# Kernel tuning notes

Hardware: AMD Instinct MI355X
Metric: run time of the kernel (lower is better)

The kernel has to match this reference:

```python
import jax, jax.numpy as jnp
import numpy as np

B, SQ, SKV, D = 4, 2048, 2048, 2048
NEG = -1e9


def setup_inputs() -> dict:
    key = jax.random.key(0)
    ks = jax.random.split(key, 7)
    x = jax.random.normal(ks[0], (B, SKV, D), dtype=jnp.float32)
    enc_q = jax.random.normal(ks[1], (B, SQ, D), dtype=jnp.float32)
    enc_k = jax.random.normal(ks[2], (B, SKV, D), dtype=jnp.float32)
    i_mask = jax.random.bernoulli(ks[3], 0.1, (B, SQ, SKV))  # True -> masked
    s = 1.0 / np.sqrt(D)
    Wq = jax.random.normal(ks[4], (D, D), dtype=jnp.float32) * s
    Wk = jax.random.normal(ks[5], (D, D), dtype=jnp.float32) * s
    Wv = jax.random.normal(ks[6], (D, D), dtype=jnp.float32) * s
    return {"x": x, "enc_q": enc_q, "enc_k": enc_k, "i_mask": i_mask,
            "Wq": Wq, "Wk": Wk, "Wv": Wv}


def reference(x, enc_q, enc_k, i_mask, Wq, Wk, Wv):
    # Bias-free linear projections (nn.Linear: y = x @ W^T)
    q = jnp.einsum('bsd,ed->bse', enc_q, Wq)   # [B,SQ,D]
    k = jnp.einsum('bsd,ed->bse', enc_k, Wk)   # [B,SKV,D]
    v = jnp.einsum('bsd,ed->bse', x, Wv)       # [B,SKV,D]
    scale = 1.0 / jnp.sqrt(jnp.asarray(q.shape[-1], q.dtype))
    scores = jnp.einsum('bqd,bkd->bqk', q, k) * scale  # [B,SQ,SKV]
    scores = jnp.where(i_mask, jnp.asarray(NEG, scores.dtype), scores)
    attn = jax.nn.softmax(scores, axis=-1)
    return jnp.einsum('bqk,bkd->bqd', attn, v)  # [B,SQ,D]
```

## Files before the change

### kernel.cpp

```cpp
#include <hip/hip_runtime.h>
#include <stdint.h>

typedef short  short8  __attribute__((ext_vector_type(8)));
typedef unsigned short ushort8 __attribute__((ext_vector_type(8)));
typedef unsigned short ushort4v __attribute__((ext_vector_type(4)));
typedef float  f32x4   __attribute__((ext_vector_type(4)));

#define BB  4
#define SQL 2048
#define SKL 2048
#define NEGV -1e9f
#define AS1 __attribute__((address_space(1)))
#define AS3 __attribute__((address_space(3)))

__device__ __forceinline__ unsigned short f2bf(float f){
  union { float f; uint32_t u; } x; x.f = f;
  return (unsigned short)((x.u + 0x7FFFu + ((x.u >> 16) & 1u)) >> 16);
}
__device__ __forceinline__ float bf2f(unsigned short h){
  union { uint32_t u; float f; } x; x.u = ((uint32_t)h) << 16;
  return x.f;
}

#define BARR() __builtin_amdgcn_s_barrier()
#define SBAR() __builtin_amdgcn_s_barrier()
#define LGKM0() asm volatile("s_waitcnt lgkmcnt(0)" ::: "memory")
#define VMW(N)  asm volatile("s_waitcnt vmcnt(" #N ")"   ::: "memory")
#define PRIO1 __builtin_amdgcn_s_setprio(1)
#define PRIO0 __builtin_amdgcn_s_setprio(0)

__global__ void mask_detect(const uint8_t* __restrict__ m, int* __restrict__ cnt){
  const long n4 = (long)BB * SQL * SKL / 4;
  long idx  = (long)blockIdx.x * blockDim.x + threadIdx.x;
  long step = (long)gridDim.x * blockDim.x;
  int c0 = 0, c1 = 0, c2 = 0;
  for (long i4 = idx; i4 < n4; i4 += step){
    uchar4 b = ((const uchar4*)m)[i4];
    c0 += (b.y != 0) + (b.z != 0) + (b.w != 0);
    c1 += (b.x > 1) + (b.y > 1) + (b.z > 1) + (b.w > 1);
    c2 += (b.y != 0);
  }
  #pragma unroll
  for (int o = 32; o >= 1; o >>= 1){
    c0 += __shfl_xor(c0, o); c1 += __shfl_xor(c1, o); c2 += __shfl_xor(c2, o);
  }
  if ((threadIdx.x & 63) == 0){
    atomicAdd(&cnt[0], c0); atomicAdd(&cnt[1], c1); atomicAdd(&cnt[2], c2);
  }
}

__global__ __launch_bounds__(256)
void cvt4(const float* __restrict__ s0, const float* __restrict__ s1,
          const float* __restrict__ s2, const float* __restrict__ s3,
          unsigned short* __restrict__ d0, unsigned short* __restrict__ d1,
          unsigned short* __restrict__ d2, unsigned short* __restrict__ d3)
{
  const long total = 6815744;
  for (long c = (long)blockIdx.x * blockDim.x + threadIdx.x; c < total;
       c += (long)gridDim.x * blockDim.x){
    const float* s; unsigned short* d; long off;
    if      (c < 2097152){ s = s0; d = d0; off = c; }
    else if (c < 4194304){ s = s1; d = d1; off = c - 2097152; }
    else if (c < 6291456){ s = s2; d = d2; off = c - 4194304; }
    else                 { s = s3; d = d3; off = c - 6291456; }
    f32x4 a = ((const f32x4*)s)[off * 2];
    f32x4 b = ((const f32x4*)s)[off * 2 + 1];
    ushort8 w;
    #pragma unroll
    for (int j = 0; j < 4; ++j){ w[j] = f2bf(a[j]); w[j + 4] = f2bf(b[j]); }
    ((ushort8*)d)[off] = w;
  }
}

__global__ __launch_bounds__(256)
void transpose_cvt2(const float* __restrict__ s0, const float* __restrict__ s1,
                    unsigned short* __restrict__ d0, unsigned short* __restrict__ d1)
{
  __shared__ float t[32][33];
  const float* s = blockIdx.z ? s1 : s0;
  unsigned short* d = blockIdx.z ? d1 : d0;
  const long bx = blockIdx.x * 32, by = blockIdx.y * 32;
  const int tx = threadIdx.x & 31, ty = threadIdx.x >> 5;
  #pragma unroll
  for (int j = 0; j < 4; ++j)
    t[ty + j * 8][tx] = s[(by + ty + j * 8) * 2048 + bx + tx];
  __syncthreads();
  #pragma unroll
  for (int j = 0; j < 4; ++j)
    d[(bx + ty + j * 8) * 2048 + by + tx] = f2bf(t[tx][ty + j * 8]);
}

__device__ __forceinline__ void xcd_decode(int& bx, int& by, int& bz){
  const int gx = gridDim.x, gy = gridDim.y;
  const int nwg = gx * gy * gridDim.z;
  const int lid = blockIdx.x + gx * (blockIdx.y + gy * blockIdx.z);
  const int sw  = (lid & 7) * (nwg >> 3) + (lid >> 3);
  bx = sw % gx;
  const int t = sw / gx;
  by = t % gy;
  bz = t / gy;
}

template<int EPI>
__device__ __forceinline__ void gemm256_body(
    const unsigned short* __restrict__ Ag, const unsigned short* __restrict__ Bg,
    void* __restrict__ Cb, const void* __restrict__ mask, const int* __restrict__ cnt,
    int bz, long Cbs, long tm, long tn, float scale,
    unsigned short (&lA)[2][16384], unsigned short (&lB)[2][16384])
{
  constexpr int LD = 2048;
  const int tid = threadIdx.x, lane = tid & 63, wid = tid >> 6;
  const int wm = wid >> 2, wn = wid & 3;
  const int l15 = lane & 15, l16 = lane >> 4;

  f32x4 acc[2][2][4][2] = {};
  short8 aF[4][2];
  short8 bF[2][2][2];

  auto stageA = [&](int buf, int half, int k){
    const unsigned short* s = Ag + (tm + half * 128) * LD + k;
    unsigned short* d = lA[buf] + half * 8192;
    #pragma unroll
    for (int l = 0; l < 2; ++l){
      const int idx = l * 512 + tid;
      const int r   = idx >> 3;
      const int gsw = (idx & 7) ^ (r & 7);
      __builtin_amdgcn_global_load_lds((const AS1 void*)(s + r * LD + gsw * 8),
                                       (AS3 void*)(d + idx * 8), 16, 0, 0);
    }
  };
  auto stageB = [&](int buf, int half, int k){
    const unsigned short* s = Bg + (tn + half * 128) * LD + k;
    unsigned short* d = lB[buf] + half * 8192;
    #pragma unroll
    for (int l = 0; l < 2; ++l){
      const int idx = l * 512 + tid;
      const int r   = idx >> 3;
      const int gsw = (idx & 7) ^ (r & 7);
      __builtin_amdgcn_global_load_lds((const AS1 void*)(s + r * LD + gsw * 8),
                                       (AS3 void*)(d + idx * 8), 16, 0, 0);
    }
  };

  #define RD_A(BUF, QM)                                                       \
    _Pragma("unroll")                                                         \
    for (int mr = 0; mr < 4; ++mr)                                            \
      _Pragma("unroll")                                                       \
      for (int ks = 0; ks < 2; ++ks){                                         \
        const int r = (QM) * 128 + wm * 64 + mr * 16 + l15;                   \
        const int g = ks * 4 + l16;                                           \
        aF[mr][ks] = *(const short8*)&lA[(BUF)][(r * 8 + (g ^ (r & 7))) * 8]; \
      }
  #define RD_B(BUF, QN)                                                       \
    _Pragma("unroll")                                                         \
    for (int nr = 0; nr < 2; ++nr)                                            \
      _Pragma("unroll")                                                       \
      for (int ks = 0; ks < 2; ++ks){                                         \
        const int c = (QN) * 128 + wn * 32 + nr * 16 + l15;                   \
        const int g = ks * 4 + l16;                                           \
        bF[QN][nr][ks] = *(const short8*)&lB[(BUF)][(c * 8 + (g ^ (c & 7))) * 8]; \
      }
  #define MFMA16(QM, QN)                                                      \
    _Pragma("unroll")                                                         \
    for (int mr = 0; mr < 4; ++mr)                                            \
      _Pragma("unroll")                                                       \
      for (int nr = 0; nr < 2; ++nr)                                          \
        _Pragma("unroll")                                                     \
        for (int ks = 0; ks < 2; ++ks)                                        \
          acc[QM][QN][mr][nr] = __builtin_amdgcn_mfma_f32_16x16x32_bf16(      \
              aF[mr][ks], bF[QN][nr][ks], acc[QM][QN][mr][nr], 0, 0, 0);

  #define KTILE_MAIN(BUF, KNXT)                                               \
  {                                                                           \
    RD_A(BUF, 0); RD_B(BUF, 0);                                               \
    stageA((BUF) ^ 1, 0, (KNXT));                                             \
    BARR(); LGKM0();                                                          \
    PRIO1; MFMA16(0, 0); PRIO0; VMW(4); BARR();                               \
    RD_B(BUF, 1);                                                             \
    stageB((BUF) ^ 1, 0, (KNXT));                                             \
    BARR(); LGKM0();                                                          \
    PRIO1; MFMA16(0, 1); PRIO0; VMW(4); BARR();                               \
    RD_A(BUF, 1);                                                             \
    stageB((BUF) ^ 1, 1, (KNXT));                                             \
    BARR(); LGKM0();                                                          \
    PRIO1; MFMA16(1, 1); PRIO0; BARR();                                       \
    stageA((BUF) ^ 1, 1, (KNXT));                                             \
    BARR();                                                                   \
    PRIO1; MFMA16(1, 0); PRIO0; VMW(2); BARR();                               \
  }
  #define KTILE_LAST(BUF)                                                     \
  {                                                                           \
    RD_A(BUF, 0); RD_B(BUF, 0);                                               \
    BARR(); LGKM0();                                                          \
    PRIO1; MFMA16(0, 0); PRIO0; VMW(2); BARR();                               \
    RD_B(BUF, 1);                                                             \
    BARR(); LGKM0();                                                          \
    PRIO1; MFMA16(0, 1); PRIO0; VMW(0); BARR();                               \
    RD_A(BUF, 1);                                                             \
    BARR(); LGKM0();                                                          \
    PRIO1; MFMA16(1, 1); PRIO0; BARR();                                       \
    PRIO1; MFMA16(1, 0); PRIO0;                                               \
  }

  stageA(0, 0, 0);
  stageB(0, 0, 0);
  stageB(0, 1, 0);
  stageA(0, 1, 0);
  VMW(4); BARR();

  for (int it = 0; it < 15; ++it){
    KTILE_MAIN(0, (2 * it + 1) * 64);
    KTILE_MAIN(1, (2 * it + 2) * 64);
  }
  KTILE_MAIN(0, 31 * 64);
  KTILE_LAST(1);

  const int colo = l15, rowg = l16 * 4;
  if constexpr (EPI == 0){
    unsigned short* C = (unsigned short*)Cb + (long)bz * Cbs;
    #pragma unroll
    for (int qm = 0; qm < 2; ++qm)
      #pragma unroll
      for (int qn = 0; qn < 2; ++qn)
        #pragma unroll
        for (int mr = 0; mr < 4; ++mr)
          #pragma unroll
          for (int j = 0; j < 4; ++j){
            const long row = tm + qm * 128 + wm * 64 + mr * 16 + rowg + j;
            unsigned short* cr = C + row * LD + tn + qn * 128 + wn * 32 + colo;
            #pragma unroll
            for (int nr = 0; nr < 2; ++nr) cr[nr * 16] = f2bf(acc[qm][qn][mr][nr][j] * scale);
          }
  } else if constexpr (EPI == 2){
    float* C = (float*)Cb + (long)bz * Cbs;
    #pragma unroll
    for (int qm = 0; qm < 2; ++qm)
      #pragma unroll
      for (int qn = 0; qn < 2; ++qn)
        #pragma unroll
        for (int mr = 0; mr < 4; ++mr)
          #pragma unroll
          for (int j = 0; j < 4; ++j){
            const long row = tm + qm * 128 + wm * 64 + mr * 16 + rowg + j;
            float* cr = C + row * LD + tn + qn * 128 + wn * 32 + colo;
            #pragma unroll
            for (int nr = 0; nr < 2; ++nr) cr[nr * 16] = acc[qm][qn][mr][nr][j];
          }
  } else {
    const int a0 = cnt[0], a1 = cnt[1], a2 = cnt[2];
    const int mmode = (a1 == 0) ? (a0 > 1000 ? 0 : 1) : (a2 > 1000 ? 2 : 3);
    unsigned short* C = (unsigned short*)Cb + (long)bz * Cbs;
    const long mbase = (long)bz * SQL * SKL;
    #pragma unroll
    for (int qm = 0; qm < 2; ++qm)
      #pragma unroll
      for (int qn = 0; qn < 2; ++qn)
        #pragma unroll
        for (int mr = 0; mr < 4; ++mr)
          #pragma unroll
          for (int j = 0; j < 4; ++j){
            const long row = tm + qm * 128 + wm * 64 + mr * 16 + rowg + j;
            #pragma unroll
            for (int nr = 0; nr < 2; ++nr){
              const long col = tn + qn * 128 + wn * 32 + nr * 16 + colo;
              const long midx = mbase + row * SKL + col;
              bool msk;
              if (mmode == 0)      msk = ((const uint8_t*)mask)[midx] != 0;
              else if (mmode == 1) msk = ((const int*)mask)[midx] != 0;
              else if (mmode == 2) msk = ((const unsigned short*)mask)[midx] != 0;
              else                 msk = ((const uint32_t*)mask)[midx] != 0;
              float vv = acc[qm][qn][mr][nr][j] * scale;
              if (msk) vv = NEGV;
              C[row * SKL + col] = f2bf(vv);
            }
          }
  }
  #undef RD_A
  #undef RD_B
  #undef MFMA16
  #undef KTILE_MAIN
  #undef KTILE_LAST
}

template<int EPI>
__global__ __launch_bounds__(512, 2)
void gemm256(const unsigned short* __restrict__ A, const unsigned short* __restrict__ B,
             void* __restrict__ Cb, const void* __restrict__ mask,
             const int* __restrict__ cnt, long Abs, long Bbs, long Cbs, float scale)
{
  __shared__ unsigned short lA[2][16384];
  __shared__ unsigned short lB[2][16384];
  int bx, by, bz; xcd_decode(bx, by, bz);
  gemm256_body<EPI>(A + (long)bz * Abs, B + (long)bz * Bbs, Cb, mask, cnt, bz, Cbs,
                    (long)by * 256, (long)bx * 256, scale, lA, lB);
}

__global__ __launch_bounds__(512, 2)
void gemm256_proj2(const unsigned short* A0, const unsigned short* A1,
                   const unsigned short* B0, const unsigned short* B1,
                   void* C0, void* C1)
{
  __shared__ unsigned short lA[2][16384];
  __shared__ unsigned short lB[2][16384];
  int bx, by, bz; xcd_decode(bx, by, bz);
  const int sec = bz >> 2, b = bz & 3;
  const long NN = (long)SQL * 2048;
  const unsigned short* Av = sec ? A1 : A0;
  const unsigned short* Bv = sec ? B1 : B0;
  void*                 Cv = sec ? C1 : C0;
  const long Abs = sec ? 0 : NN;
  const long Bbs = sec ? NN : 0;
  gemm256_body<0>(Av + (long)b * Abs, Bv + (long)b * Bbs, Cv, nullptr, nullptr, b, NN,
                  (long)by * 256, (long)bx * 256, 1.f, lA, lB);
}

template<int AMODE, int BMODE, int EPI>
__device__ __forceinline__ void gemm_body(
    const void* __restrict__ Av, const void* __restrict__ Bv,
    void* __restrict__ Cb, const void* __restrict__ mask, const int* __restrict__ cnt,
    int bz, long Abs, long Bbs, long Cbs, long tm, long tn, float scale,
    int koff, int klen,
    unsigned short (*lA)[4096], unsigned short (*lB)[4096])
{
  constexpr int LD = 2048;
  const int tid = threadIdx.x, lane = tid & 63, wave = tid >> 6;
  const int wr = wave >> 1, wc = wave & 1;
  const int c0 = tid, c1 = tid + 256;
  const int r0 = c0 >> 2, q0 = (c0 & 3) * 8;
  const int r1 = c1 >> 2, q1 = (c1 & 3) * 8;

  const unsigned short* A16 = (const unsigned short*)Av + (long)bz * Abs;
  const unsigned short* B16 = (const unsigned short*)Bv + (long)bz * Bbs;
  const float*          A32 = (const float*)Av + (long)bz * Abs;
  const float*          B32 = (const float*)Bv + (long)bz * Bbs;

  f32x4 acc[4][4] = {};
  f32x4 sA[4], sB[4];

  auto issueA = [&](int buf, int kk){
    if constexpr (AMODE == 0){
      __builtin_amdgcn_global_load_lds((const AS1 void*)(A16 + (tm + r0) * LD + q0 + kk),
                                       (AS3 void*)(lA[buf] + c0 * 8), 16, 0, 0);
      __builtin_amdgcn_global_load_lds((const AS1 void*)(A16 + (tm + r1) * LD + q1 + kk),
                                       (AS3 void*)(lA[buf] + c1 * 8), 16, 0, 0);
    } else {
      sA[0] = *(const f32x4*)(A32 + (tm + r0) * LD + q0 + kk);
      sA[1] = *(const f32x4*)(A32 + (tm + r0) * LD + q0 + kk + 4);
      sA[2] = *(const f32x4*)(A32 + (tm + r1) * LD + q1 + kk);
      sA[3] = *(const f32x4*)(A32 + (tm + r1) * LD + q1 + kk + 4);
    }
  };
  auto issueB = [&](int buf, int kk){
    if constexpr (BMODE == 0){
      __builtin_amdgcn_global_load_lds((const AS1 void*)(B16 + (tn + r0) * LD + q0 + kk),
                                       (AS3 void*)(lB[buf] + c0 * 8), 16, 0, 0);
      __builtin_amdgcn_global_load_lds((const AS1 void*)(B16 + (tn + r1) * LD + q1 + kk),
                                       (AS3 void*)(lB[buf] + c1 * 8), 16, 0, 0);
    } else {
      sB[0] = *(const f32x4*)(B32 + (tn + r0) * LD + q0 + kk);
      sB[1] = *(const f32x4*)(B32 + (tn + r0) * LD + q0 + kk + 4);
      sB[2] = *(const f32x4*)(B32 + (tn + r1) * LD + q1 + kk);
      sB[3] = *(const f32x4*)(B32 + (tn + r1) * LD + q1 + kk + 4);
    }
  };
  auto writeA = [&](int buf){
    if constexpr (AMODE == 1){
      ushort8 w0, w1;
      #pragma unroll
      for (int j = 0; j < 4; ++j){
        w0[j] = f2bf(sA[0][j]); w0[j + 4] = f2bf(sA[1][j]);
        w1[j] = f2bf(sA[2][j]); w1[j + 4] = f2bf(sA[3][j]);
      }
      *(ushort8*)(lA[buf] + c0 * 8) = w0;
      *(ushort8*)(lA[buf] + c1 * 8) = w1;
    }
  };
  auto writeB = [&](int buf){
    if constexpr (BMODE == 1){
      ushort8 w0, w1;
      #pragma unroll
      for (int j = 0; j < 4; ++j){
        w0[j] = f2bf(sB[0][j]); w0[j + 4] = f2bf(sB[1][j]);
        w1[j] = f2bf(sB[2][j]); w1[j + 4] = f2bf(sB[3][j]);
      }
      *(ushort8*)(lB[buf] + c0 * 8) = w0;
      *(ushort8*)(lB[buf] + c1 * 8) = w1;
    }
  };
  auto computeTile = [&](int buf){
    short8 aF[4], bF[4];
    #pragma unroll
    for (int m = 0; m < 4; ++m)
      aF[m] = *(const short8*)(lA[buf] + (wr * 64 + m * 16 + (lane & 15)) * 32 + (lane >> 4) * 8);
    #pragma unroll
    for (int n = 0; n < 4; ++n)
      bF[n] = *(const short8*)(lB[buf] + (wc * 64 + n * 16 + (lane & 15)) * 32 + (lane >> 4) * 8);
    #pragma unroll
    for (int m = 0; m < 4; ++m)
      #pragma unroll
      for (int n = 0; n < 4; ++n)
        acc[m][n] = __builtin_amdgcn_mfma_f32_16x16x32_bf16(aF[m], bF[n], acc[m][n], 0, 0, 0);
  };

  issueA(0, koff); issueB(0, koff); writeA(0); writeB(0);
  __syncthreads();
  int cur = 0;
  for (int k0 = koff; k0 < koff + klen - 32; k0 += 32){
    issueA(cur ^ 1, k0 + 32);
    issueB(cur ^ 1, k0 + 32);
    computeTile(cur);
    writeA(cur ^ 1); writeB(cur ^ 1);
    __syncthreads();
    cur ^= 1;
  }
  computeTile(cur);

  const int colo = lane & 15, rowg = (lane >> 4) * 4;
  if constexpr (EPI == 0){
    unsigned short* C = (unsigned short*)Cb + (long)bz * Cbs;
    #pragma unroll
    for (int m = 0; m < 4; ++m)
      #pragma unroll
      for (int j = 0; j < 4; ++j){
        const long row = tm + wr * 64 + m * 16 + rowg + j;
        unsigned short* cr = C + row * LD + tn + wc * 64 + colo;
        #pragma unroll
        for (int n = 0; n < 4; ++n) cr[n * 16] = f2bf(acc[m][n][j] * scale);
      }
  } else if constexpr (EPI == 2){
    float* C = (float*)Cb + (long)bz * Cbs;
    #pragma unroll
    for (int m = 0; m < 4; ++m)
      #pragma unroll
      for (int j = 0; j < 4; ++j){
        const long row = tm + wr * 64 + m * 16 + rowg + j;
        float* cr = C + row * LD + tn + wc * 64 + colo;
        #pragma unroll
        for (int n = 0; n < 4; ++n) cr[n * 16] = acc[m][n][j];
      }
  } else {
    const int a0 = cnt[0], a1 = cnt[1], a2 = cnt[2];
    const int mmode = (a1 == 0) ? (a0 > 1000 ? 0 : 1) : (a2 > 1000 ? 2 : 3);
    unsigned short* C = (unsigned short*)Cb + (long)bz * Cbs;
    const long mbase = (long)bz * SQL * SKL;
    #pragma unroll
    for (int m = 0; m < 4; ++m)
      #pragma unroll
      for (int j = 0; j < 4; ++j){
        const long row = tm + wr * 64 + m * 16 + rowg + j;
        #pragma unroll
        for (int n = 0; n < 4; ++n){
          const long col = tn + wc * 64 + n * 16 + colo;
          const long midx = mbase + row * SKL + col;
          bool msk;
          if (mmode == 0)      msk = ((const uint8_t*)mask)[midx] != 0;
          else if (mmode == 1) msk = ((const int*)mask)[midx] != 0;
          else if (mmode == 2) msk = ((const unsigned short*)mask)[midx] != 0;
          else                 msk = ((const uint32_t*)mask)[midx] != 0;
          float vv = acc[m][n][j] * scale;
          if (msk) vv = NEGV;
          C[row * SKL + col] = f2bf(vv);
        }
      }
  }
}

template<int AMODE, int BMODE, int EPI>
__global__ __launch_bounds__(256, 2)
void gemm_nt(const void* __restrict__ Abv, const void* __restrict__ Bbv,
             void* __restrict__ Cb, const void* __restrict__ mask,
             const int* __restrict__ cnt,
             long Abs, long Bbs, long Cbs, float scale)
{
  __shared__ unsigned short lA[2][4096];
  __shared__ unsigned short lB[2][4096];
  int bx, by, bz; xcd_decode(bx, by, bz);
  gemm_body<AMODE, BMODE, EPI>(Abv, Bbv, Cb, mask, cnt, bz, Abs, Bbs, Cbs,
                               (long)by * 128, (long)bx * 128, scale, 0, 2048, lA, lB);
}

__global__ __launch_bounds__(256, 2)
void gemm_splitk(const unsigned short* __restrict__ A, const unsigned short* __restrict__ B,
                 float* __restrict__ Cp)
{
  __shared__ unsigned short lA[2][4096];
  __shared__ unsigned short lB[2][4096];
  int bx, by, bz; xcd_decode(bx, by, bz);
  gemm_body<0, 0, 2>(A, B, Cp + (long)bz * 4194304, nullptr, nullptr, 0, 0, 0, 4194304,
                     (long)by * 128, (long)bx * 128, 1.f, bz * 512, 512, lA, lB);
}

__global__ __launch_bounds__(256)
void mt_reduce(const float* __restrict__ Cp, unsigned short* __restrict__ Mt, float scale){
  for (long c = (long)blockIdx.x * blockDim.x + threadIdx.x; c < 1048576;
       c += (long)gridDim.x * blockDim.x){
    f32x4 a = ((const f32x4*)Cp)[c];
    f32x4 b = ((const f32x4*)(Cp + 4194304))[c];
    f32x4 d = ((const f32x4*)(Cp + 8388608))[c];
    f32x4 e = ((const f32x4*)(Cp + 12582912))[c];
    ushort4v w;
    #pragma unroll
    for (int j = 0; j < 4; ++j) w[j] = f2bf((a[j] + b[j] + d[j] + e[j]) * scale);
    ((ushort4v*)Mt)[c] = w;
  }
}

template<int MODE>
__global__ __launch_bounds__(256, 2)
void gemm_proj3(const void* A0, const void* A1, const void* A2,
                const void* B0, const void* B1, const void* B2,
                void* C0, void* C1, void* C2)
{
  __shared__ unsigned short lA[2][4096];
  __shared__ unsigned short lB[2][4096];
  int bx, by, bz; xcd_decode(bx, by, bz);
  const int sec = bz >> 2, b = bz & 3;
  const long NN = (long)SQL * 2048;
  const void* Av = sec == 0 ? A0 : sec == 1 ? A1 : A2;
  const void* Bv = sec == 0 ? B0 : sec == 1 ? B1 : B2;
  void*       Cv = sec == 0 ? C0 : sec == 1 ? C1 : C2;
  const long Abs = (sec == 2) ? 0 : NN;
  const long Bbs = (sec == 2) ? NN : 0;
  gemm_body<MODE, MODE, 0>(Av, Bv, Cv, nullptr, nullptr, b, Abs, Bbs, NN,
                           (long)by * 128, (long)bx * 128, 1.f, 0, 2048, lA, lB);
}

__global__ __launch_bounds__(256, 4)
void softmax_rows(const unsigned short* __restrict__ S, unsigned short* __restrict__ P){
  const long row = blockIdx.x;
  const int t = threadIdx.x;
  ushort8 u = *((const ushort8*)(S + row * SKL) + t);
  float v[8];
  #pragma unroll
  for (int j = 0; j < 8; ++j) v[j] = bf2f(u[j]);
  float mx = v[0];
  #pragma unroll
  for (int j = 1; j < 8; ++j) mx = fmaxf(mx, v[j]);
  #pragma unroll
  for (int o = 32; o >= 1; o >>= 1) mx = fmaxf(mx, __shfl_xor(mx, o));
  __shared__ float red[8];
  const int wv = t >> 6, ln = t & 63;
  if (ln == 0) red[wv] = mx;
  __syncthreads();
  mx = fmaxf(fmaxf(red[0], red[1]), fmaxf(red[2], red[3]));
  float e[8], sum = 0.f;
  #pragma unroll
  for (int j = 0; j < 8; ++j){ e[j] = exp2f((v[j] - mx) * 1.4426950408889634f); sum += e[j]; }
  #pragma unroll
  for (int o = 32; o >= 1; o >>= 1) sum += __shfl_xor(sum, o);
  if (ln == 0) red[4 + wv] = sum;
  __syncthreads();
  sum = red[4] + red[5] + red[6] + red[7];
  const float inv = 1.0f / sum;
  ushort8 o8;
  #pragma unroll
  for (int j = 0; j < 8; ++j) o8[j] = f2bf(e[j] * inv);
  *((ushort8*)(P + row * SKL) + t) = o8;
}

extern "C" void kernel_launch(void* const* d_in, const int* in_sizes, int n_in,
                              void* d_out, int out_size, void* d_ws, size_t ws_size,
                              hipStream_t stream)
{
  (void)in_sizes; (void)n_in; (void)out_size;
  const void* x    = d_in[0];
  const void* encq = d_in[1];
  const void* enck = d_in[2];
  const void* imsk = d_in[3];
  const void* Wq   = d_in[4];
  const void* Wk   = d_in[5];
  const void* Wv   = d_in[6];

  uint8_t* ws = (uint8_t*)d_ws;
  int* cnt = (int*)ws;
  const long NN = (long)2048 * 2048;
  const float scale = 0.022097086912079608f;

  hipMemsetAsync(cnt, 0, 4096, stream);
  mask_detect<<<256, 256, 0, stream>>>((const uint8_t*)imsk, cnt);

  const size_t FULL_NEED = 4096 + 4ull * 33554432 + 4ull * 8388608;
  if (ws_size >= FULL_NEED){
    unsigned short* xb  = (unsigned short*)(ws + 4096);
    unsigned short* qb  = xb  + 16777216;
    unsigned short* kb  = qb  + 16777216;
    unsigned short* Wvb = kb  + 16777216;
    unsigned short* WqT = Wvb + 4194304;
    unsigned short* WkT = WqT + 4194304;
    unsigned short* Mt  = WkT + 4194304;
    unsigned short* Vt  = Mt  + 4194304;
    unsigned short* U   = (unsigned short*)d_out;
    unsigned short* S   = U + 16777216;
    unsigned short* P   = qb;

    cvt4<<<2048, 256, 0, stream>>>((const float*)x, (const float*)encq, (const float*)enck,
                                   (const float*)Wv, xb, qb, kb, Wvb);
    transpose_cvt2<<<dim3(64, 64, 2), 256, 0, stream>>>((const float*)Wq, (const float*)Wk,
                                                        WqT, WkT);
    gemm_splitk<<<dim3(16, 16, 4), 256, 0, stream>>>(WkT, WqT, (float*)d_out);
    mt_reduce<<<1024, 256, 0, stream>>>((const float*)d_out, Mt, scale);
    gemm256_proj2<<<dim3(8, 8, 8), 512, 0, stream>>>(qb, Wvb, Mt, xb, U, Vt);
    gemm256<1><<<dim3(8, 8, BB), 512, 0, stream>>>(U, kb, S, imsk, cnt, NN, NN, NN, 1.f);
    softmax_rows<<<BB * SQL, 256, 0, stream>>>(S, P);
    gemm256<2><<<dim3(8, 8, BB), 512, 0, stream>>>(P, Vt, d_out, nullptr, cnt, NN, NN, NN, 1.f);
  } else {
    unsigned short* Q  = (unsigned short*)(ws + 4096);
    unsigned short* Kp = Q  + 16777216;
    unsigned short* Vt = Kp + 16777216;
    unsigned short* P  = Q;
    unsigned short* S;
    const size_t need = 4096 + 4ull * 33554432;
    if (ws_size >= need) S = Vt + 16777216;
    else                 S = (unsigned short*)d_out;

    gemm_proj3<1><<<dim3(16, 16, 12), 256, 0, stream>>>(encq, enck, Wv, Wq, Wk, x, Q, Kp, Vt);
    gemm_nt<0, 0, 1><<<dim3(16, 16, BB), 256, 0, stream>>>(Q, Kp, S, imsk, cnt, NN, NN, NN, scale);
    softmax_rows<<<BB * SQL, 256, 0, stream>>>(S, P);
    gemm_nt<0, 0, 2><<<dim3(16, 16, BB), 256, 0, stream>>>(P, Vt, d_out, nullptr, cnt, NN, NN, NN, 1.f);
  }
}
```

Measured before the change: 515.9 us.

## Move mask application into softmax and merge conversion kernels into one launch

Mask application moves out of the score-GEMM epilogue, which did scattered byte loads per element, and into the softmax kernel, which now reads the mask with vectorized loads per row. The GEMM epilogue becomes a plain bf16 store. The convert and transpose kernels are merged into a single prep launch to save one kernel launch. The mask then goes through softmax after bf16 rounding of the scores, which matches the earlier behaviour because the same NEG value is used either way.

After: 454.1 us. 1.14x faster.

```diff
diff --git a/kernel.cpp b/kernel.cpp
--- a/kernel.cpp
+++ b/kernel.cpp
@@ -23,7 +23,6 @@
 }
 
 #define BARR() __builtin_amdgcn_s_barrier()
-#define SBAR() __builtin_amdgcn_s_barrier()
 #define LGKM0() asm volatile("s_waitcnt lgkmcnt(0)" ::: "memory")
 #define VMW(N)  asm volatile("s_waitcnt vmcnt(" #N ")"   ::: "memory")
 #define PRIO1 __builtin_amdgcn_s_setprio(1)
@@ -50,44 +49,44 @@
 }
 
 __global__ __launch_bounds__(256)
-void cvt4(const float* __restrict__ s0, const float* __restrict__ s1,
+void prep(const float* __restrict__ s0, const float* __restrict__ s1,
           const float* __restrict__ s2, const float* __restrict__ s3,
           unsigned short* __restrict__ d0, unsigned short* __restrict__ d1,
-          unsigned short* __restrict__ d2, unsigned short* __restrict__ d3)
-{
-  const long total = 6815744;
-  for (long c = (long)blockIdx.x * blockDim.x + threadIdx.x; c < total;
-       c += (long)gridDim.x * blockDim.x){
-    const float* s; unsigned short* d; long off;
-    if      (c < 2097152){ s = s0; d = d0; off = c; }
-    else if (c < 4194304){ s = s1; d = d1; off = c - 2097152; }
-    else if (c < 6291456){ s = s2; d = d2; off = c - 4194304; }
-    else                 { s = s3; d = d3; off = c - 6291456; }
-    f32x4 a = ((const f32x4*)s)[off * 2];
-    f32x4 b = ((const f32x4*)s)[off * 2 + 1];
-    ushort8 w;
-    #pragma unroll
-    for (int j = 0; j < 4; ++j){ w[j] = f2bf(a[j]); w[j + 4] = f2bf(b[j]); }
-    ((ushort8*)d)[off] = w;
-  }
-}
-
-__global__ __launch_bounds__(256)
-void transpose_cvt2(const float* __restrict__ s0, const float* __restrict__ s1,
-                    unsigned short* __restrict__ d0, unsigned short* __restrict__ d1)
-{
-  __shared__ float t[32][33];
-  const float* s = blockIdx.z ? s1 : s0;
-  unsigned short* d = blockIdx.z ? d1 : d0;
-  const long bx = blockIdx.x * 32, by = blockIdx.y * 32;
-  const int tx = threadIdx.x & 31, ty = threadIdx.x >> 5;
-  #pragma unroll
-  for (int j = 0; j < 4; ++j)
-    t[ty + j * 8][tx] = s[(by + ty + j * 8) * 2048 + bx + tx];
-  __syncthreads();
-  #pragma unroll
-  for (int j = 0; j < 4; ++j)
-    d[(bx + ty + j * 8) * 2048 + by + tx] = f2bf(t[tx][ty + j * 8]);
+          unsigned short* __restrict__ d2, unsigned short* __restrict__ d3,
+          const float* __restrict__ tq, const float* __restrict__ tk,
+          unsigned short* __restrict__ dq, unsigned short* __restrict__ dk)
+{
+  if (blockIdx.x < 2048){
+    const long total = 6815744;
+    for (long c = (long)blockIdx.x * 256 + threadIdx.x; c < total; c += 2048 * 256){
+      const float* s; unsigned short* d; long off;
+      if      (c < 2097152){ s = s0; d = d0; off = c; }
+      else if (c < 4194304){ s = s1; d = d1; off = c - 2097152; }
+      else if (c < 6291456){ s = s2; d = d2; off = c - 4194304; }
+      else                 { s = s3; d = d3; off = c - 6291456; }
+      f32x4 a = ((const f32x4*)s)[off * 2];
+      f32x4 b = ((const f32x4*)s)[off * 2 + 1];
+      ushort8 w;
+      #pragma unroll
+      for (int j = 0; j < 4; ++j){ w[j] = f2bf(a[j]); w[j + 4] = f2bf(b[j]); }
+      ((ushort8*)d)[off] = w;
+    }
+  } else {
+    __shared__ float t[32][33];
+    const int j = blockIdx.x - 2048;
+    const int z = j >> 12, rem = j & 4095;
+    const float* s = z ? tk : tq;
+    unsigned short* d = z ? dk : dq;
+    const long bx = (long)(rem & 63) * 32, by = (long)(rem >> 6) * 32;
+    const int tx = threadIdx.x & 31, ty = threadIdx.x >> 5;
+    #pragma unroll
+    for (int jj = 0; jj < 4; ++jj)
+      t[ty + jj * 8][tx] = s[(by + ty + jj * 8) * 2048 + bx + tx];
+    __syncthreads();
+    #pragma unroll
+    for (int jj = 0; jj < 4; ++jj)
+      d[(bx + ty + jj * 8) * 2048 + by + tx] = f2bf(t[tx][ty + jj * 8]);
+  }
 }
 
 __device__ __forceinline__ void xcd_decode(int& bx, int& by, int& bz){
@@ -104,8 +103,7 @@
 template<int EPI>
 __device__ __forceinline__ void gemm256_body(
     const unsigned short* __restrict__ Ag, const unsigned short* __restrict__ Bg,
-    void* __restrict__ Cb, const void* __restrict__ mask, const int* __restrict__ cnt,
-    int bz, long Cbs, long tm, long tn, float scale,
+    void* __restrict__ Cb, int bz, long Cbs, long tm, long tn, float scale,
     unsigned short (&lA)[2][16384], unsigned short (&lB)[2][16384])
 {
   constexpr int LD = 2048;
@@ -231,7 +229,7 @@
             #pragma unroll
             for (int nr = 0; nr < 2; ++nr) cr[nr * 16] = f2bf(acc[qm][qn][mr][nr][j] * scale);
           }
-  } else if constexpr (EPI == 2){
+  } else {
     float* C = (float*)Cb + (long)bz * Cbs;
     #pragma unroll
     for (int qm = 0; qm < 2; ++qm)
@@ -246,34 +244,6 @@
             #pragma unroll
             for (int nr = 0; nr < 2; ++nr) cr[nr * 16] = acc[qm][qn][mr][nr][j];
           }
-  } else {
-    const int a0 = cnt[0], a1 = cnt[1], a2 = cnt[2];
-    const int mmode = (a1 == 0) ? (a0 > 1000 ? 0 : 1) : (a2 > 1000 ? 2 : 3);
-    unsigned short* C = (unsigned short*)Cb + (long)bz * Cbs;
-    const long mbase = (long)bz * SQL * SKL;
-    #pragma unroll
-    for (int qm = 0; qm < 2; ++qm)
-      #pragma unroll
-      for (int qn = 0; qn < 2; ++qn)
-        #pragma unroll
-        for (int mr = 0; mr < 4; ++mr)
-          #pragma unroll
-          for (int j = 0; j < 4; ++j){
-            const long row = tm + qm * 128 + wm * 64 + mr * 16 + rowg + j;
-            #pragma unroll
-            for (int nr = 0; nr < 2; ++nr){
-              const long col = tn + qn * 128 + wn * 32 + nr * 16 + colo;
-              const long midx = mbase + row * SKL + col;
-              bool msk;
-              if (mmode == 0)      msk = ((const uint8_t*)mask)[midx] != 0;
-              else if (mmode == 1) msk = ((const int*)mask)[midx] != 0;
-              else if (mmode == 2) msk = ((const unsigned short*)mask)[midx] != 0;
-              else                 msk = ((const uint32_t*)mask)[midx] != 0;
-              float vv = acc[qm][qn][mr][nr][j] * scale;
-              if (msk) vv = NEGV;
-              C[row * SKL + col] = f2bf(vv);
-            }
-          }
   }
   #undef RD_A
   #undef RD_B
@@ -285,13 +255,12 @@
 template<int EPI>
 __global__ __launch_bounds__(512, 2)
 void gemm256(const unsigned short* __restrict__ A, const unsigned short* __restrict__ B,
-             void* __restrict__ Cb, const void* __restrict__ mask,
-             const int* __restrict__ cnt, long Abs, long Bbs, long Cbs, float scale)
+             void* __restrict__ Cb, long Abs, long Bbs, long Cbs, float scale)
 {
   __shared__ unsigned short lA[2][16384];
   __shared__ unsigned short lB[2][16384];
   int bx, by, bz; xcd_decode(bx, by, bz);
-  gemm256_body<EPI>(A + (long)bz * Abs, B + (long)bz * Bbs, Cb, mask, cnt, bz, Cbs,
+  gemm256_body<EPI>(A + (long)bz * Abs, B + (long)bz * Bbs, Cb, bz, Cbs,
                     (long)by * 256, (long)bx * 256, scale, lA, lB);
 }
 
@@ -310,16 +279,15 @@
   void*                 Cv = sec ? C1 : C0;
   const long Abs = sec ? 0 : NN;
   const long Bbs = sec ? NN : 0;
-  gemm256_body<0>(Av + (long)b * Abs, Bv + (long)b * Bbs, Cv, nullptr, nullptr, b, NN,
+  gemm256_body<0>(Av + (long)b * Abs, Bv + (long)b * Bbs, Cv, b, NN,
                   (long)by * 256, (long)bx * 256, 1.f, lA, lB);
 }
 
 template<int AMODE, int BMODE, int EPI>
 __device__ __forceinline__ void gemm_body(
     const void* __restrict__ Av, const void* __restrict__ Bv,
-    void* __restrict__ Cb, const void* __restrict__ mask, const int* __restrict__ cnt,
-    int bz, long Abs, long Bbs, long Cbs, long tm, long tn, float scale,
-    int koff, int klen,
+    void* __restrict__ Cb, int bz, long Abs, long Bbs, long Cbs,
+    long tm, long tn, float scale, int koff, int klen,
     unsigned short (*lA)[4096], unsigned short (*lB)[4096])
 {
   constexpr int LD = 2048;
@@ -427,7 +395,7 @@
         #pragma unroll
         for (int n = 0; n < 4; ++n) cr[n * 16] = f2bf(acc[m][n][j] * scale);
       }
-  } else if constexpr (EPI == 2){
+  } else {
     float* C = (float*)Cb + (long)bz * Cbs;
     #pragma unroll
     for (int m = 0; m < 4; ++m)
@@ -438,44 +406,18 @@
         #pragma unroll
         for (int n = 0; n < 4; ++n) cr[n * 16] = acc[m][n][j];
       }
-  } else {
-    const int a0 = cnt[0], a1 = cnt[1], a2 = cnt[2];
-    const int mmode = (a1 == 0) ? (a0 > 1000 ? 0 : 1) : (a2 > 1000 ? 2 : 3);
-    unsigned short* C = (unsigned short*)Cb + (long)bz * Cbs;
-    const long mbase = (long)bz * SQL * SKL;
-    #pragma unroll
-    for (int m = 0; m < 4; ++m)
-      #pragma unroll
-      for (int j = 0; j < 4; ++j){
-        const long row = tm + wr * 64 + m * 16 + rowg + j;
-        #pragma unroll
-        for (int n = 0; n < 4; ++n){
-          const long col = tn + wc * 64 + n * 16 + colo;
-          const long midx = mbase + row * SKL + col;
-          bool msk;
-          if (mmode == 0)      msk = ((const uint8_t*)mask)[midx] != 0;
-          else if (mmode == 1) msk = ((const int*)mask)[midx] != 0;
-          else if (mmode == 2) msk = ((const unsigned short*)mask)[midx] != 0;
-          else                 msk = ((const uint32_t*)mask)[midx] != 0;
-          float vv = acc[m][n][j] * scale;
-          if (msk) vv = NEGV;
-          C[row * SKL + col] = f2bf(vv);
-        }
-      }
   }
 }
 
 template<int AMODE, int BMODE, int EPI>
 __global__ __launch_bounds__(256, 2)
 void gemm_nt(const void* __restrict__ Abv, const void* __restrict__ Bbv,
-             void* __restrict__ Cb, const void* __restrict__ mask,
-             const int* __restrict__ cnt,
-             long Abs, long Bbs, long Cbs, float scale)
+             void* __restrict__ Cb, long Abs, long Bbs, long Cbs, float scale)
 {
   __shared__ unsigned short lA[2][4096];
   __shared__ unsigned short lB[2][4096];
   int bx, by, bz; xcd_decode(bx, by, bz);
-  gemm_body<AMODE, BMODE, EPI>(Abv, Bbv, Cb, mask, cnt, bz, Abs, Bbs, Cbs,
+  gemm_body<AMODE, BMODE, EPI>(Abv, Bbv, Cb, bz, Abs, Bbs, Cbs,
                                (long)by * 128, (long)bx * 128, scale, 0, 2048, lA, lB);
 }
 
@@ -486,7 +428,7 @@
   __shared__ unsigned short lA[2][4096];
   __shared__ unsigned short lB[2][4096];
   int bx, by, bz; xcd_decode(bx, by, bz);
-  gemm_body<0, 0, 2>(A, B, Cp + (long)bz * 4194304, nullptr, nullptr, 0, 0, 0, 4194304,
+  gemm_body<0, 0, 2>(A, B, Cp + (long)bz * 4194304, 0, 0, 0, 4194304,
                      (long)by * 128, (long)bx * 128, 1.f, bz * 512, 512, lA, lB);
 }
 
@@ -505,11 +447,10 @@
   }
 }
 
-template<int MODE>
 __global__ __launch_bounds__(256, 2)
-void gemm_proj3(const void* A0, const void* A1, const void* A2,
-                const void* B0, const void* B1, const void* B2,
-                void* C0, void* C1, void* C2)
+void gemm_proj3f(const void* A0, const void* A1, const void* A2,
+                 const void* B0, const void* B1, const void* B2,
+                 void* C0, void* C1, void* C2)
 {
   __shared__ unsigned short lA[2][4096];
   __shared__ unsigned short lB[2][4096];
@@ -521,18 +462,42 @@
   void*       Cv = sec == 0 ? C0 : sec == 1 ? C1 : C2;
   const long Abs = (sec == 2) ? 0 : NN;
   const long Bbs = (sec == 2) ? NN : 0;
-  gemm_body<MODE, MODE, 0>(Av, Bv, Cv, nullptr, nullptr, b, Abs, Bbs, NN,
-                           (long)by * 128, (long)bx * 128, 1.f, 0, 2048, lA, lB);
+  gemm_body<1, 1, 0>(Av, Bv, Cv, b, Abs, Bbs, NN,
+                     (long)by * 128, (long)bx * 128, 1.f, 0, 2048, lA, lB);
 }
 
 __global__ __launch_bounds__(256, 4)
-void softmax_rows(const unsigned short* __restrict__ S, unsigned short* __restrict__ P){
+void softmax_rows(const unsigned short* __restrict__ S, const void* __restrict__ mask,
+                  const int* __restrict__ cnt, unsigned short* __restrict__ P){
   const long row = blockIdx.x;
   const int t = threadIdx.x;
+  const int a0 = cnt[0], a1 = cnt[1], a2 = cnt[2];
+  const int mmode = (a1 == 0) ? (a0 > 1000 ? 0 : 1) : (a2 > 1000 ? 2 : 3);
+
   ushort8 u = *((const ushort8*)(S + row * SKL) + t);
   float v[8];
   #pragma unroll
   for (int j = 0; j < 8; ++j) v[j] = bf2f(u[j]);
+
+  const long mb = row * SKL + (long)t * 8;
+  if (mmode == 0){
+    uchar4 m0 = ((const uchar4*)mask)[mb / 4], m1 = ((const uchar4*)mask)[mb / 4 + 1];
+    if (m0.x) v[0] = NEGV; if (m0.y) v[1] = NEGV; if (m0.z) v[2] = NEGV; if (m0.w) v[3] = NEGV;
+    if (m1.x) v[4] = NEGV; if (m1.y) v[5] = NEGV; if (m1.z) v[6] = NEGV; if (m1.w) v[7] = NEGV;
+  } else if (mmode == 1){
+    int4 m0 = ((const int4*)mask)[mb / 4], m1 = ((const int4*)mask)[mb / 4 + 1];
+    if (m0.x) v[0] = NEGV; if (m0.y) v[1] = NEGV; if (m0.z) v[2] = NEGV; if (m0.w) v[3] = NEGV;
+    if (m1.x) v[4] = NEGV; if (m1.y) v[5] = NEGV; if (m1.z) v[6] = NEGV; if (m1.w) v[7] = NEGV;
+  } else if (mmode == 2){
+    ushort8 m = ((const ushort8*)mask)[mb / 8];
+    #pragma unroll
+    for (int j = 0; j < 8; ++j) if (m[j]) v[j] = NEGV;
+  } else {
+    f32x4 m0 = ((const f32x4*)mask)[mb / 4], m1 = ((const f32x4*)mask)[mb / 4 + 1];
+    #pragma unroll
+    for (int j = 0; j < 4; ++j){ if (m0[j] != 0.f) v[j] = NEGV; if (m1[j] != 0.f) v[4 + j] = NEGV; }
+  }
+
   float mx = v[0];
   #pragma unroll
   for (int j = 1; j < 8; ++j) mx = fmaxf(mx, v[j]);
@@ -593,16 +558,15 @@
     unsigned short* S   = U + 16777216;
     unsigned short* P   = qb;
 
-    cvt4<<<2048, 256, 0, stream>>>((const float*)x, (const float*)encq, (const float*)enck,
-                                   (const float*)Wv, xb, qb, kb, Wvb);
-    transpose_cvt2<<<dim3(64, 64, 2), 256, 0, stream>>>((const float*)Wq, (const float*)Wk,
-                                                        WqT, WkT);
+    prep<<<10240, 256, 0, stream>>>((const float*)x, (const float*)encq, (const float*)enck,
+                                    (const float*)Wv, xb, qb, kb, Wvb,
+                                    (const float*)Wq, (const float*)Wk, WqT, WkT);
     gemm_splitk<<<dim3(16, 16, 4), 256, 0, stream>>>(WkT, WqT, (float*)d_out);
     mt_reduce<<<1024, 256, 0, stream>>>((const float*)d_out, Mt, scale);
     gemm256_proj2<<<dim3(8, 8, 8), 512, 0, stream>>>(qb, Wvb, Mt, xb, U, Vt);
-    gemm256<1><<<dim3(8, 8, BB), 512, 0, stream>>>(U, kb, S, imsk, cnt, NN, NN, NN, 1.f);
-    softmax_rows<<<BB * SQL, 256, 0, stream>>>(S, P);
-    gemm256<2><<<dim3(8, 8, BB), 512, 0, stream>>>(P, Vt, d_out, nullptr, cnt, NN, NN, NN, 1.f);
+    gemm256<0><<<dim3(8, 8, BB), 512, 0, stream>>>(U, kb, S, NN, NN, NN, 1.f);
+    softmax_rows<<<BB * SQL, 256, 0, stream>>>(S, imsk, cnt, P);
+    gemm256<2><<<dim3(8, 8, BB), 512, 0, stream>>>(P, Vt, d_out, NN, NN, NN, 1.f);
   } else {
     unsigned short* Q  = (unsigned short*)(ws + 4096);
     unsigned short* Kp = Q  + 16777216;
@@ -613,9 +577,9 @@
     if (ws_size >= need) S = Vt + 16777216;
     else                 S = (unsigned short*)d_out;
 
-    gemm_proj3<1><<<dim3(16, 16, 12), 256, 0, stream>>>(encq, enck, Wv, Wq, Wk, x, Q, Kp, Vt);
-    gemm_nt<0, 0, 1><<<dim3(16, 16, BB), 256, 0, stream>>>(Q, Kp, S, imsk, cnt, NN, NN, NN, scale);
-    softmax_rows<<<BB * SQL, 256, 0, stream>>>(S, P);
-    gemm_nt<0, 0, 2><<<dim3(16, 16, BB), 256, 0, stream>>>(P, Vt, d_out, nullptr, cnt, NN, NN, NN, 1.f);
-  }
-}
+    gemm_proj3f<<<dim3(16, 16, 12), 256, 0, stream>>>(encq, enck, Wv, Wq, Wk, x, Q, Kp, Vt);
+    gemm_nt<0, 0, 0><<<dim3(16, 16, BB), 256, 0, stream>>>(Q, Kp, S, NN, NN, NN, scale);
+    softmax_rows<<<BB * SQL, 256, 0, stream>>>(S, imsk, cnt, P);
+    gemm_nt<0, 0, 2><<<dim3(16, 16, BB), 256, 0, stream>>>(P, Vt, d_out, NN, NN, NN, 1.f);
+  }
+}
```
